# Performance work log

Measured on AMD Instinct MI355X. Metric: run time of the kernel, lower is better.

Reference implementation:

```python
import jax, jax.numpy as jnp
import numpy as np

B = 512      # batch size
D = 128      # per-input feature dim (hard-coded as 2*128 in the torch module)
H = 512      # hidden_dim


def setup_inputs() -> dict:
    key = jax.random.key(0)
    kx, ky, kw1, kw2 = jax.random.split(key, 4)
    x = jax.random.normal(kx, (B, D), dtype=jnp.float32)
    y = jax.random.normal(ky, (B, D), dtype=jnp.float32)
    # Linear layer params (torch Linear default-ish init scale)
    W1 = jax.random.normal(kw1, (2 * D, H), dtype=jnp.float32) * (1.0 / np.sqrt(2 * D))
    b1 = jnp.zeros((H,), dtype=jnp.float32)
    W2 = jax.random.normal(kw2, (H, 1), dtype=jnp.float32) * (1.0 / np.sqrt(H))
    b2 = jnp.zeros((1,), dtype=jnp.float32)
    return {"x": x, "y": y, "W1": W1, "b1": b1, "W2": W2, "b2": b2}


def reference(x, y, W1, b1, W2, b2):
    # Faithful to torch: pairs[i, j] = concat(x[j], y[i])
    b = x.shape[0]
    x_t = jnp.broadcast_to(x[None, :, :], (b, b, x.shape[1]))   # tile x along dim 0
    y_t = jnp.broadcast_to(y[:, None, :], (b, b, y.shape[1]))   # tile y along dim 1
    pairs = jnp.concatenate([x_t, y_t], axis=2).reshape(b * b, 2 * x.shape[1])  # [B*B, 2D]
    h = jax.nn.relu(pairs @ W1 + b1)          # [B*B, H]
    scores = h @ W2 + b2                       # [B*B, 1]
    # reshape to (B, B) then transpose, as in torch.t(...)
    # result[a, b] = mlp(concat(x[a], y[b]))
    return scores.reshape(b, b).T
```

## Files before the change

kernel.cpp:

```cpp
#include <hip/hip_runtime.h>
#include <hip/hip_bf16.h>


#define B 512
#define D 128
#define H 512
#define CH 64
#define LDP 68

__global__ __launch_bounds__(256) void k1_uv(
        const float* __restrict__ x, const float* __restrict__ y,
        const float* __restrict__ W1, const float* __restrict__ b1,
        const float* __restrict__ W2,
        float* __restrict__ U, float* __restrict__ V, float* __restrict__ PQ) {
    const int m  = blockIdx.y;
    const int z  = blockIdx.z;
    const int a0 = blockIdx.x * 4;
    const float* __restrict__ src = (m == 0) ? x : y;
    float* __restrict__ dst       = (m == 0) ? U : V;
    const float* __restrict__ Wm  = W1 + (size_t)m * D * H;

    __shared__ float xs[4][D];
    __shared__ float red[4][4];
    const int t = threadIdx.x;
    for (int i = t; i < 4 * D; i += 256)
        xs[i >> 7][i & (D - 1)] = src[(size_t)(a0 + (i >> 7)) * D + (i & (D - 1))];
    __syncthreads();

    const int h = z * 256 + t;
    float bias = (m == 0) ? b1[h] : 0.0f;
    float acc[4] = {bias, bias, bias, bias};
#pragma unroll 4
    for (int d = 0; d < D; ++d) {
        const float w = Wm[(size_t)d * H + h];
#pragma unroll
        for (int r = 0; r < 4; ++r) acc[r] = fmaf(xs[r][d], w, acc[r]);
    }
#pragma unroll
    for (int r = 0; r < 4; ++r) dst[(size_t)(a0 + r) * H + h] = acc[r];

    const float wp = 0.5f * W2[h];
    float v[4];
#pragma unroll
    for (int r = 0; r < 4; ++r) v[r] = acc[r] * wp;
#pragma unroll
    for (int r = 0; r < 4; ++r)
        for (int o = 32; o > 0; o >>= 1) v[r] += __shfl_down(v[r], o);
    const int wave = t >> 6;
    if ((t & 63) == 0)
#pragma unroll
        for (int r = 0; r < 4; ++r) red[wave][r] = v[r];
    __syncthreads();
    if (t < 4) {
        const float s = red[0][t] + red[1][t] + red[2][t] + red[3][t];
        PQ[(size_t)(m * 2 + z) * B + a0 + t] = s;
    }
}

__global__ __launch_bounds__(256) void k2_pair(
        const float* __restrict__ U, const float* __restrict__ V,
        const float* __restrict__ W2, float* __restrict__ P, int hcount) {
    __shared__ float Us[CH][LDP];
    __shared__ float Vs[CH][LDP];

    const int a0 = blockIdx.x * 64;
    const int b0 = blockIdx.y * 64;
    const int h0 = blockIdx.z * hcount;
    const int tid = threadIdx.x;
    const int ta = tid & 15;
    const int tb = tid >> 4;
    const int r = tid >> 2;
    const int q = tid & 3;

    float acc[4][4] = {};

    for (int c = 0; c < hcount; c += CH) {
        const float* __restrict__ Urow = U + (size_t)(a0 + r) * H + h0 + c;
        const float* __restrict__ Vrow = V + (size_t)(b0 + r) * H + h0 + c;
#pragma unroll
        for (int p = 0; p < 4; ++p) {
            const int hh = 4 * q + 16 * p;
            const float4 u4 = *(const float4*)(Urow + hh);
            const float4 v4 = *(const float4*)(Vrow + hh);
            Us[hh + 0][r] = u4.x; Us[hh + 1][r] = u4.y;
            Us[hh + 2][r] = u4.z; Us[hh + 3][r] = u4.w;
            Vs[hh + 0][r] = v4.x; Vs[hh + 1][r] = v4.y;
            Vs[hh + 2][r] = v4.z; Vs[hh + 3][r] = v4.w;
        }
        __syncthreads();

#pragma unroll 4
        for (int hh = 0; hh < CH; ++hh) {
            const float w = W2[h0 + c + hh];
            const float4 ua = *(const float4*)&Us[hh][4 * ta];
            const float4 vb = *(const float4*)&Vs[hh][4 * tb];
            const float u[4] = {ua.x, ua.y, ua.z, ua.w};
            const float v[4] = {vb.x, vb.y, vb.z, vb.w};
#pragma unroll
            for (int i = 0; i < 4; ++i)
#pragma unroll
                for (int j = 0; j < 4; ++j)
                    acc[i][j] = fmaf(__builtin_fabsf(u[i] + v[j]), w, acc[i][j]);
        }
        __syncthreads();
    }

    float* __restrict__ out = P + (size_t)blockIdx.z * (B * B);
#pragma unroll
    for (int i = 0; i < 4; ++i) {
        float4 o;
        o.x = acc[i][0]; o.y = acc[i][1]; o.z = acc[i][2]; o.w = acc[i][3];
        *(float4*)(out + (size_t)(a0 + 4 * ta + i) * B + b0 + 4 * tb) = o;
    }
}

__global__ __launch_bounds__(256) void k3_reduce(
        const float* __restrict__ Pp, const float* __restrict__ PQ,
        const float* __restrict__ b2, float* __restrict__ out, int S) {
    const int gi = blockIdx.x * 256 + threadIdx.x;
    const int i = gi * 4;
    const int a = i >> 9;
    const int b = i & (B - 1);

    float4 s = {0.f, 0.f, 0.f, 0.f};
    for (int z = 0; z < S; ++z) {
        const float4 p = *(const float4*)(Pp + (size_t)z * (B * B) + i);
        s.x += p.x; s.y += p.y; s.z += p.z; s.w += p.w;
    }
    const float pa = PQ[a] + PQ[B + a] + b2[0];
    const float4 qb0 = *(const float4*)(PQ + 2 * B + b);
    const float4 qb1 = *(const float4*)(PQ + 3 * B + b);
    float4 o;
    o.x = pa + qb0.x + qb1.x + 0.5f * s.x;
    o.y = pa + qb0.y + qb1.y + 0.5f * s.y;
    o.z = pa + qb0.z + qb1.z + 0.5f * s.z;
    o.w = pa + qb0.w + qb1.w + 0.5f * s.w;
    *(float4*)(out + i) = o;
}

extern "C" void kernel_launch(void* const* d_in, const int* in_sizes, int n_in,
                              void* d_out, int out_size, void* d_ws, size_t ws_size,
                              hipStream_t stream) {
    const float* x  = (const float*)d_in[0];
    const float* y  = (const float*)d_in[1];
    const float* W1 = (const float*)d_in[2];
    const float* b1 = (const float*)d_in[3];
    const float* W2 = (const float*)d_in[4];
    const float* b2 = (const float*)d_in[5];
    float* out = (float*)d_out;

    float* U  = (float*)d_ws;
    float* V  = U + (size_t)B * H;
    float* PQ = V + (size_t)B * H;
    float* Pp = PQ + 4 * B;

    const size_t base = (2ull * B * H + 4 * B) * sizeof(float);
    int S = 1;
    if (ws_size >= base + 8ull * B * B * sizeof(float)) S = 8;
    else if (ws_size >= base + 4ull * B * B * sizeof(float)) S = 4;
    else if (ws_size >= base + 2ull * B * B * sizeof(float)) S = 2;

    k1_uv<<<dim3(B / 4, 2, 2), 256, 0, stream>>>(x, y, W1, b1, W2, U, V, PQ);
    k2_pair<<<dim3(8, 8, S), 256, 0, stream>>>(U, V, W2, Pp, H / S);
    k3_reduce<<<dim3((B * B) / (256 * 4)), 256, 0, stream>>>(Pp, PQ, b2, out, S);
}
```

Baseline: 31.69 us.

## Fuse split-H reduction into pair kernel via last-block atomic counter

Removes the separate reduce kernel. Each pair block writes its partial tile and bumps a per-tile atomic counter, and the last of the 8 split-H blocks sums the partials and writes the final output. The counters are reset inside the first kernel. The split is now fixed at 8 with no workspace-size check, W2 is staged in shared memory, and the first kernel's unroll goes from 4 to 8. This saves one launch and a full pass over the partial buffers. In exchange it uses scalar atomic stores and loads instead of float4, and relies on relaxed atomics plus a waitcnt for visibility, which is a correctness risk.

New measurement: 43.17 us. 1.36x slower.

```diff
diff --git a/kernel.cpp b/kernel.cpp
--- a/kernel.cpp
+++ b/kernel.cpp
@@ -12,25 +12,30 @@
         const float* __restrict__ x, const float* __restrict__ y,
         const float* __restrict__ W1, const float* __restrict__ b1,
         const float* __restrict__ W2,
-        float* __restrict__ U, float* __restrict__ V, float* __restrict__ PQ) {
+        float* __restrict__ U, float* __restrict__ V, float* __restrict__ PQ,
+        int* __restrict__ cnt) {
     const int m  = blockIdx.y;
     const int z  = blockIdx.z;
     const int a0 = blockIdx.x * 4;
+    const int t = threadIdx.x;
+
+    if (blockIdx.x == 0 && m == 0 && z == 0 && t < 64)
+        __hip_atomic_store(&cnt[t], 0, __ATOMIC_RELAXED, __HIP_MEMORY_SCOPE_AGENT);
+
     const float* __restrict__ src = (m == 0) ? x : y;
     float* __restrict__ dst       = (m == 0) ? U : V;
     const float* __restrict__ Wm  = W1 + (size_t)m * D * H;
 
     __shared__ float xs[4][D];
     __shared__ float red[4][4];
-    const int t = threadIdx.x;
     for (int i = t; i < 4 * D; i += 256)
         xs[i >> 7][i & (D - 1)] = src[(size_t)(a0 + (i >> 7)) * D + (i & (D - 1))];
     __syncthreads();
 
     const int h = z * 256 + t;
-    float bias = (m == 0) ? b1[h] : 0.0f;
+    const float bias = (m == 0) ? b1[h] : 0.0f;
     float acc[4] = {bias, bias, bias, bias};
-#pragma unroll 4
+#pragma unroll 8
     for (int d = 0; d < D; ++d) {
         const float w = Wm[(size_t)d * H + h];
 #pragma unroll
@@ -57,85 +62,92 @@
     }
 }
 
-__global__ __launch_bounds__(256) void k2_pair(
+__global__ __launch_bounds__(256) void k2_fused(
         const float* __restrict__ U, const float* __restrict__ V,
-        const float* __restrict__ W2, float* __restrict__ P, int hcount) {
+        const float* __restrict__ W2, const float* __restrict__ PQ,
+        const float* __restrict__ b2, float* __restrict__ Pp,
+        int* __restrict__ cnt, float* __restrict__ out) {
     __shared__ float Us[CH][LDP];
     __shared__ float Vs[CH][LDP];
+    __shared__ float w2s[CH];
+    __shared__ int lastFlag;
 
     const int a0 = blockIdx.x * 64;
     const int b0 = blockIdx.y * 64;
-    const int h0 = blockIdx.z * hcount;
-    const int tid = threadIdx.x;
-    const int ta = tid & 15;
-    const int tb = tid >> 4;
-    const int r = tid >> 2;
-    const int q = tid & 3;
+    const int zp = blockIdx.z;
+    const int h0 = zp * CH;
+    const int t = threadIdx.x;
+    const int ta = t & 15;
+    const int tb = t >> 4;
+    const int r = t >> 2;
+    const int q = t & 3;
+
+    const float* __restrict__ Urow = U + (size_t)(a0 + r) * H + h0;
+    const float* __restrict__ Vrow = V + (size_t)(b0 + r) * H + h0;
+#pragma unroll
+    for (int p = 0; p < 4; ++p) {
+        const int hh = 4 * q + 16 * p;
+        const float4 u4 = *(const float4*)(Urow + hh);
+        const float4 v4 = *(const float4*)(Vrow + hh);
+        Us[hh + 0][r] = u4.x; Us[hh + 1][r] = u4.y;
+        Us[hh + 2][r] = u4.z; Us[hh + 3][r] = u4.w;
+        Vs[hh + 0][r] = v4.x; Vs[hh + 1][r] = v4.y;
+        Vs[hh + 2][r] = v4.z; Vs[hh + 3][r] = v4.w;
+    }
+    if (t < CH) w2s[t] = W2[h0 + t];
+    __syncthreads();
 
     float acc[4][4] = {};
-
-    for (int c = 0; c < hcount; c += CH) {
-        const float* __restrict__ Urow = U + (size_t)(a0 + r) * H + h0 + c;
-        const float* __restrict__ Vrow = V + (size_t)(b0 + r) * H + h0 + c;
+#pragma unroll 4
+    for (int hh = 0; hh < CH; ++hh) {
+        const float w = w2s[hh];
+        const float4 ua = *(const float4*)&Us[hh][4 * ta];
+        const float4 vb = *(const float4*)&Vs[hh][4 * tb];
+        const float u[4] = {ua.x, ua.y, ua.z, ua.w};
+        const float v[4] = {vb.x, vb.y, vb.z, vb.w};
 #pragma unroll
-        for (int p = 0; p < 4; ++p) {
-            const int hh = 4 * q + 16 * p;
-            const float4 u4 = *(const float4*)(Urow + hh);
-            const float4 v4 = *(const float4*)(Vrow + hh);
-            Us[hh + 0][r] = u4.x; Us[hh + 1][r] = u4.y;
-            Us[hh + 2][r] = u4.z; Us[hh + 3][r] = u4.w;
-            Vs[hh + 0][r] = v4.x; Vs[hh + 1][r] = v4.y;
-            Vs[hh + 2][r] = v4.z; Vs[hh + 3][r] = v4.w;
-        }
-        __syncthreads();
-
-#pragma unroll 4
-        for (int hh = 0; hh < CH; ++hh) {
-            const float w = W2[h0 + c + hh];
-            const float4 ua = *(const float4*)&Us[hh][4 * ta];
-            const float4 vb = *(const float4*)&Vs[hh][4 * tb];
-            const float u[4] = {ua.x, ua.y, ua.z, ua.w};
-            const float v[4] = {vb.x, vb.y, vb.z, vb.w};
+        for (int i = 0; i < 4; ++i)
 #pragma unroll
-            for (int i = 0; i < 4; ++i)
-#pragma unroll
-                for (int j = 0; j < 4; ++j)
-                    acc[i][j] = fmaf(__builtin_fabsf(u[i] + v[j]), w, acc[i][j]);
-        }
-        __syncthreads();
+            for (int j = 0; j < 4; ++j)
+                acc[i][j] = fmaf(__builtin_fabsf(u[i] + v[j]), w, acc[i][j]);
     }
 
-    float* __restrict__ out = P + (size_t)blockIdx.z * (B * B);
+    float* __restrict__ outp = Pp + (size_t)zp * (B * B);
 #pragma unroll
-    for (int i = 0; i < 4; ++i) {
-        float4 o;
-        o.x = acc[i][0]; o.y = acc[i][1]; o.z = acc[i][2]; o.w = acc[i][3];
-        *(float4*)(out + (size_t)(a0 + 4 * ta + i) * B + b0 + 4 * tb) = o;
+    for (int i = 0; i < 4; ++i)
+#pragma unroll
+        for (int j = 0; j < 4; ++j)
+            __hip_atomic_store(&outp[(size_t)(a0 + 4 * ta + i) * B + b0 + 4 * tb + j],
+                               acc[i][j], __ATOMIC_RELAXED, __HIP_MEMORY_SCOPE_AGENT);
+
+    asm volatile("s_waitcnt vmcnt(0)" ::: "memory");
+    __syncthreads();
+    if (t == 0) {
+        const int old = __hip_atomic_fetch_add(&cnt[blockIdx.y * 8 + blockIdx.x], 1,
+                                               __ATOMIC_RELAXED, __HIP_MEMORY_SCOPE_AGENT);
+        lastFlag = (old == 7);
     }
-}
+    __syncthreads();
 
-__global__ __launch_bounds__(256) void k3_reduce(
-        const float* __restrict__ Pp, const float* __restrict__ PQ,
-        const float* __restrict__ b2, float* __restrict__ out, int S) {
-    const int gi = blockIdx.x * 256 + threadIdx.x;
-    const int i = gi * 4;
-    const int a = i >> 9;
-    const int b = i & (B - 1);
-
-    float4 s = {0.f, 0.f, 0.f, 0.f};
-    for (int z = 0; z < S; ++z) {
-        const float4 p = *(const float4*)(Pp + (size_t)z * (B * B) + i);
-        s.x += p.x; s.y += p.y; s.z += p.z; s.w += p.w;
+    if (lastFlag) {
+        const int a = a0 + 4 * ta;
+        const int b = b0 + 4 * tb;
+        const float bb = b2[0];
+#pragma unroll
+        for (int i = 0; i < 4; ++i) {
+            const float pa = PQ[a + i] + PQ[B + a + i] + bb;
+#pragma unroll
+            for (int j = 0; j < 4; ++j) {
+                float s = 0.0f;
+#pragma unroll
+                for (int zz = 0; zz < 8; ++zz)
+                    s += __hip_atomic_load(&Pp[(size_t)zz * (B * B) + (size_t)(a + i) * B + b + j],
+                                           __ATOMIC_RELAXED, __HIP_MEMORY_SCOPE_AGENT);
+                const float qb = PQ[2 * B + b + j] + PQ[3 * B + b + j];
+                out[(size_t)(a + i) * B + b + j] = pa + qb + 0.5f * s;
+            }
+        }
     }
-    const float pa = PQ[a] + PQ[B + a] + b2[0];
-    const float4 qb0 = *(const float4*)(PQ + 2 * B + b);
-    const float4 qb1 = *(const float4*)(PQ + 3 * B + b);
-    float4 o;
-    o.x = pa + qb0.x + qb1.x + 0.5f * s.x;
-    o.y = pa + qb0.y + qb1.y + 0.5f * s.y;
-    o.z = pa + qb0.z + qb1.z + 0.5f * s.z;
-    o.w = pa + qb0.w + qb1.w + 0.5f * s.w;
-    *(float4*)(out + i) = o;
 }
 
 extern "C" void kernel_launch(void* const* d_in, const int* in_sizes, int n_in,
@@ -149,18 +161,12 @@
     const float* b2 = (const float*)d_in[5];
     float* out = (float*)d_out;
 
-    float* U  = (float*)d_ws;
+    int* cnt  = (int*)d_ws;
+    float* U  = (float*)((char*)d_ws + 1024);
     float* V  = U + (size_t)B * H;
     float* PQ = V + (size_t)B * H;
     float* Pp = PQ + 4 * B;
 
-    const size_t base = (2ull * B * H + 4 * B) * sizeof(float);
-    int S = 1;
-    if (ws_size >= base + 8ull * B * B * sizeof(float)) S = 8;
-    else if (ws_size >= base + 4ull * B * B * sizeof(float)) S = 4;
-    else if (ws_size >= base + 2ull * B * B * sizeof(float)) S = 2;
-
-    k1_uv<<<dim3(B / 4, 2, 2), 256, 0, stream>>>(x, y, W1, b1, W2, U, V, PQ);
-    k2_pair<<<dim3(8, 8, S), 256, 0, stream>>>(U, V, W2, Pp, H / S);
-    k3_reduce<<<dim3((B * B) / (256 * 4)), 256, 0, stream>>>(Pp, PQ, b2, out, S);
+    k1_uv<<<dim3(B / 4, 2, 2), 256, 0, stream>>>(x, y, W1, b1, W2, U, V, PQ, cnt);
+    k2_fused<<<dim3(8, 8, 8), 256, 0, stream>>>(U, V, W2, PQ, b2, Pp, cnt, out);
 }
```

## Restructure first-layer kernel with float4 weight loads and fix split-H count at four

Applied to the files above, without the earlier changes.

The first kernel now has each thread compute four hidden columns using float4 weight loads. The D reduction is split across two thread halves and combined through shared memory, so the grid's z dimension is no longer needed. The pair kernel keeps the 0.5*W2 values in shared memory instead of reading them from global memory in the inner loop. The split count S is now fixed at 4 rather than chosen from the workspace size, so the pair kernel runs 256 blocks and the reduction reads four partial buffers. This trades the old adaptive split (possibly 8) for fewer partials and cheaper reduction traffic, but it drops the workspace-size check.

Measured after the change: 34.61 us. 1.09x slower.

```diff
diff --git a/kernel.cpp b/kernel.cpp
--- a/kernel.cpp
+++ b/kernel.cpp
@@ -7,6 +7,7 @@
 #define H 512
 #define CH 64
 #define LDP 68
+#define S 4
 
 __global__ __launch_bounds__(256) void k1_uv(
         const float* __restrict__ x, const float* __restrict__ y,
@@ -14,63 +15,96 @@
         const float* __restrict__ W2,
         float* __restrict__ U, float* __restrict__ V, float* __restrict__ PQ) {
     const int m  = blockIdx.y;
-    const int z  = blockIdx.z;
     const int a0 = blockIdx.x * 4;
+    const int t  = threadIdx.x;
+    const int p  = t >> 7;
+    const int s4 = t & 127;
+    const int h  = s4 * 4;
+
     const float* __restrict__ src = (m == 0) ? x : y;
     float* __restrict__ dst       = (m == 0) ? U : V;
     const float* __restrict__ Wm  = W1 + (size_t)m * D * H;
 
     __shared__ float xs[4][D];
-    __shared__ float red[4][4];
-    const int t = threadIdx.x;
+    __shared__ float mred[16][128];
+    __shared__ float red2[2][4];
+
     for (int i = t; i < 4 * D; i += 256)
         xs[i >> 7][i & (D - 1)] = src[(size_t)(a0 + (i >> 7)) * D + (i & (D - 1))];
     __syncthreads();
 
-    const int h = z * 256 + t;
-    float bias = (m == 0) ? b1[h] : 0.0f;
-    float acc[4] = {bias, bias, bias, bias};
-#pragma unroll 4
-    for (int d = 0; d < D; ++d) {
-        const float w = Wm[(size_t)d * H + h];
+    float acc[4][4] = {};
+#pragma unroll 8
+    for (int dd = 0; dd < D; dd += 2) {
+        const int d = dd + p;
+        const float4 w4 = *(const float4*)(Wm + (size_t)d * H + h);
 #pragma unroll
-        for (int r = 0; r < 4; ++r) acc[r] = fmaf(xs[r][d], w, acc[r]);
+        for (int r = 0; r < 4; ++r) {
+            const float xv = xs[r][d];
+            acc[r][0] = fmaf(xv, w4.x, acc[r][0]);
+            acc[r][1] = fmaf(xv, w4.y, acc[r][1]);
+            acc[r][2] = fmaf(xv, w4.z, acc[r][2]);
+            acc[r][3] = fmaf(xv, w4.w, acc[r][3]);
+        }
     }
+
+    if (p == 1)
 #pragma unroll
-    for (int r = 0; r < 4; ++r) dst[(size_t)(a0 + r) * H + h] = acc[r];
+        for (int r = 0; r < 4; ++r)
+#pragma unroll
+            for (int c = 0; c < 4; ++c) mred[r * 4 + c][s4] = acc[r][c];
+    __syncthreads();
 
-    const float wp = 0.5f * W2[h];
-    float v[4];
+    if (p == 0) {
 #pragma unroll
-    for (int r = 0; r < 4; ++r) v[r] = acc[r] * wp;
+        for (int r = 0; r < 4; ++r)
 #pragma unroll
-    for (int r = 0; r < 4; ++r)
-        for (int o = 32; o > 0; o >>= 1) v[r] += __shfl_down(v[r], o);
-    const int wave = t >> 6;
-    if ((t & 63) == 0)
+            for (int c = 0; c < 4; ++c) acc[r][c] += mred[r * 4 + c][s4];
+        if (m == 0) {
+            const float4 bb = *(const float4*)(b1 + h);
 #pragma unroll
-        for (int r = 0; r < 4; ++r) red[wave][r] = v[r];
+            for (int r = 0; r < 4; ++r) {
+                acc[r][0] += bb.x; acc[r][1] += bb.y;
+                acc[r][2] += bb.z; acc[r][3] += bb.w;
+            }
+        }
+#pragma unroll
+        for (int r = 0; r < 4; ++r) {
+            float4 o; o.x = acc[r][0]; o.y = acc[r][1]; o.z = acc[r][2]; o.w = acc[r][3];
+            *(float4*)(dst + (size_t)(a0 + r) * H + h) = o;
+        }
+        const float4 w2 = *(const float4*)(W2 + h);
+        float v[4];
+#pragma unroll
+        for (int r = 0; r < 4; ++r)
+            v[r] = 0.5f * (acc[r][0] * w2.x + acc[r][1] * w2.y +
+                           acc[r][2] * w2.z + acc[r][3] * w2.w);
+#pragma unroll
+        for (int r = 0; r < 4; ++r)
+            for (int o = 32; o > 0; o >>= 1) v[r] += __shfl_down(v[r], o);
+        if ((t & 63) == 0)
+#pragma unroll
+            for (int r = 0; r < 4; ++r) red2[t >> 6][r] = v[r];
+    }
     __syncthreads();
-    if (t < 4) {
-        const float s = red[0][t] + red[1][t] + red[2][t] + red[3][t];
-        PQ[(size_t)(m * 2 + z) * B + a0 + t] = s;
-    }
+    if (t < 4) PQ[(size_t)m * B + a0 + t] = red2[0][t] + red2[1][t];
 }
 
 __global__ __launch_bounds__(256) void k2_pair(
         const float* __restrict__ U, const float* __restrict__ V,
-        const float* __restrict__ W2, float* __restrict__ P, int hcount) {
+        const float* __restrict__ W2, float* __restrict__ Pp, int hcount) {
     __shared__ float Us[CH][LDP];
     __shared__ float Vs[CH][LDP];
+    __shared__ float w2s[CH];
 
     const int a0 = blockIdx.x * 64;
     const int b0 = blockIdx.y * 64;
     const int h0 = blockIdx.z * hcount;
-    const int tid = threadIdx.x;
-    const int ta = tid & 15;
-    const int tb = tid >> 4;
-    const int r = tid >> 2;
-    const int q = tid & 3;
+    const int t  = threadIdx.x;
+    const int ta = t & 15;
+    const int tb = t >> 4;
+    const int r  = t >> 2;
+    const int q  = t & 3;
 
     float acc[4][4] = {};
 
@@ -78,8 +112,8 @@
         const float* __restrict__ Urow = U + (size_t)(a0 + r) * H + h0 + c;
         const float* __restrict__ Vrow = V + (size_t)(b0 + r) * H + h0 + c;
 #pragma unroll
-        for (int p = 0; p < 4; ++p) {
-            const int hh = 4 * q + 16 * p;
+        for (int pp = 0; pp < 4; ++pp) {
+            const int hh = 4 * q + 16 * pp;
             const float4 u4 = *(const float4*)(Urow + hh);
             const float4 v4 = *(const float4*)(Vrow + hh);
             Us[hh + 0][r] = u4.x; Us[hh + 1][r] = u4.y;
@@ -87,11 +121,12 @@
             Vs[hh + 0][r] = v4.x; Vs[hh + 1][r] = v4.y;
             Vs[hh + 2][r] = v4.z; Vs[hh + 3][r] = v4.w;
         }
+        if (t < CH) w2s[t] = 0.5f * W2[h0 + c + t];
         __syncthreads();
 
 #pragma unroll 4
         for (int hh = 0; hh < CH; ++hh) {
-            const float w = W2[h0 + c + hh];
+            const float w = w2s[hh];
             const float4 ua = *(const float4*)&Us[hh][4 * ta];
             const float4 vb = *(const float4*)&Vs[hh][4 * tb];
             const float u[4] = {ua.x, ua.y, ua.z, ua.w};
@@ -105,36 +140,36 @@
         __syncthreads();
     }
 
-    float* __restrict__ out = P + (size_t)blockIdx.z * (B * B);
+    float* __restrict__ outp = Pp + (size_t)blockIdx.z * (B * B);
 #pragma unroll
     for (int i = 0; i < 4; ++i) {
         float4 o;
         o.x = acc[i][0]; o.y = acc[i][1]; o.z = acc[i][2]; o.w = acc[i][3];
-        *(float4*)(out + (size_t)(a0 + 4 * ta + i) * B + b0 + 4 * tb) = o;
+        *(float4*)(outp + (size_t)(a0 + 4 * ta + i) * B + b0 + 4 * tb) = o;
     }
 }
 
 __global__ __launch_bounds__(256) void k3_reduce(
         const float* __restrict__ Pp, const float* __restrict__ PQ,
-        const float* __restrict__ b2, float* __restrict__ out, int S) {
+        const float* __restrict__ b2, float* __restrict__ out) {
     const int gi = blockIdx.x * 256 + threadIdx.x;
     const int i = gi * 4;
     const int a = i >> 9;
     const int b = i & (B - 1);
 
     float4 s = {0.f, 0.f, 0.f, 0.f};
+#pragma unroll
     for (int z = 0; z < S; ++z) {
         const float4 p = *(const float4*)(Pp + (size_t)z * (B * B) + i);
         s.x += p.x; s.y += p.y; s.z += p.z; s.w += p.w;
     }
-    const float pa = PQ[a] + PQ[B + a] + b2[0];
-    const float4 qb0 = *(const float4*)(PQ + 2 * B + b);
-    const float4 qb1 = *(const float4*)(PQ + 3 * B + b);
+    const float pa = PQ[a] + b2[0];
+    const float4 qb = *(const float4*)(PQ + B + b);
     float4 o;
-    o.x = pa + qb0.x + qb1.x + 0.5f * s.x;
-    o.y = pa + qb0.y + qb1.y + 0.5f * s.y;
-    o.z = pa + qb0.z + qb1.z + 0.5f * s.z;
-    o.w = pa + qb0.w + qb1.w + 0.5f * s.w;
+    o.x = pa + qb.x + s.x;
+    o.y = pa + qb.y + s.y;
+    o.z = pa + qb.z + s.z;
+    o.w = pa + qb.w + s.w;
     *(float4*)(out + i) = o;
 }
 
@@ -152,15 +187,9 @@
     float* U  = (float*)d_ws;
     float* V  = U + (size_t)B * H;
     float* PQ = V + (size_t)B * H;
-    float* Pp = PQ + 4 * B;
+    float* Pp = PQ + 2 * B;
 
-    const size_t base = (2ull * B * H + 4 * B) * sizeof(float);
-    int S = 1;
-    if (ws_size >= base + 8ull * B * B * sizeof(float)) S = 8;
-    else if (ws_size >= base + 4ull * B * B * sizeof(float)) S = 4;
-    else if (ws_size >= base + 2ull * B * B * sizeof(float)) S = 2;
-
-    k1_uv<<<dim3(B / 4, 2, 2), 256, 0, stream>>>(x, y, W1, b1, W2, U, V, PQ);
+    k1_uv<<<dim3(B / 4, 2), 256, 0, stream>>>(x, y, W1, b1, W2, U, V, PQ);
     k2_pair<<<dim3(8, 8, S), 256, 0, stream>>>(U, V, W2, Pp, H / S);
-    k3_reduce<<<dim3((B * B) / (256 * 4)), 256, 0, stream>>>(Pp, PQ, b2, out, S);
+    k3_reduce<<<dim3((B * B) / (256 * 4)), 256, 0, stream>>>(Pp, PQ, b2, out);
 }
```
